# Kernel optimization log

Hardware: AMD Instinct MI355X
Metric: run time of the kernel (lower is better)

Reference implementation:

```python
import jax, jax.numpy as jnp
import numpy as np

NUM_CLASSES = 2
TOP_K = 1500
CONF_THRESH = 0.01
NMS_THRESH = 0.2
VAR0, VAR1 = 0.1, 0.2  # cfg['variance']


def setup_inputs() -> dict:
    key = jax.random.key(0)
    k1, k2, k3 = jax.random.split(key, 3)
    B, P = 32, 76800
    loc_data = jax.random.normal(k1, (B, P, 4), jnp.float32)
    conf_data = jax.random.uniform(k2, (B * P, NUM_CLASSES), jnp.float32)
    prior_data = jax.random.uniform(k3, (P, 4), jnp.float32)
    return {"loc_data": loc_data, "conf_data": conf_data, "prior_data": prior_data}


def _decode(loc, priors):
    # loc, priors: [P,4]; SSD box decode with variances
    cxcy = priors[:, :2] + loc[:, :2] * VAR0 * priors[:, 2:]
    wh = priors[:, 2:] * jnp.exp(loc[:, 2:] * VAR1)
    x1y1 = cxcy - wh * 0.5
    return jnp.concatenate([x1y1, x1y1 + wh], axis=-1)  # [P,4] (x1,y1,x2,y2)


def _nms_per_class(scores, boxes):
    # scores: [P], boxes: [P,4] -> [TOP_K,5] packed (score,x1,y1,x2,y2)
    s = jnp.where(scores > CONF_THRESH, scores, -jnp.inf)
    sk, idx = jax.lax.top_k(s, TOP_K)  # torch nms keeps only top_k candidates
    bk = boxes[idx]
    x1, y1, x2, y2 = bk[:, 0], bk[:, 1], bk[:, 2], bk[:, 3]
    area = (x2 - x1) * (y2 - y1)
    iota = jnp.arange(TOP_K)

    def step(active, i):
        # greedy NMS over score-descending candidates
        xx1 = jnp.maximum(x1, x1[i]); yy1 = jnp.maximum(y1, y1[i])
        xx2 = jnp.minimum(x2, x2[i]); yy2 = jnp.minimum(y2, y2[i])
        inter = jnp.maximum(xx2 - xx1, 0.0) * jnp.maximum(yy2 - yy1, 0.0)
        iou = inter / (area + area[i] - inter)
        kept = active[i]
        suppress = (iou > NMS_THRESH) & (iota != i)
        active = jnp.where(kept, active & ~suppress, active)
        return active, kept

    _, keep = jax.lax.scan(step, sk > -jnp.inf, iota)
    rows = jnp.where(keep[:, None], jnp.concatenate([sk[:, None], bk], axis=1), 0.0)
    # pack kept rows at the front (score-descending order), zeros after
    rank = jnp.cumsum(keep) - 1
    dest = jnp.where(keep, rank, TOP_K)  # dump non-kept into scratch slot
    return jnp.zeros((TOP_K + 1, 5), bk.dtype).at[dest].set(rows)[:TOP_K]


def reference(loc_data, conf_data, prior_data):
    B, P, _ = loc_data.shape
    conf = conf_data.reshape(B, P, NUM_CLASSES)
    decoded = jax.vmap(_decode, in_axes=(0, None))(loc_data, prior_data)  # [B,P,4]
    outs = []
    for cl in range(1, NUM_CLASSES):  # background class 0 stays zero
        outs.append(jax.vmap(_nms_per_class)(conf[:, :, cl], decoded))
    bg = jnp.zeros((B, 1, TOP_K, 5), decoded.dtype)
    return jnp.concatenate([bg, jnp.stack(outs, axis=1)], axis=1)  # [B,C,TOP_K,5]
```

## Files before the change

kernel.cpp:

```cpp
#include <hip/hip_runtime.h>
#include <stdint.h>

typedef unsigned long long u64;
typedef unsigned int u32;

#define NUM_B 32
#define NUM_P 76800
#define TOPK 1500
#define NBINS 2048
#define CAP 2048
#define NWORDS 24
#define NCHUNK 6
#define HSLICES 16
#define HCHUNK (NUM_P / HSLICES)

__device__ __forceinline__ u32 fbits(float f) { return __float_as_uint(f); }
__device__ __forceinline__ int binOf(float s) {
    int b = (int)(s * (float)NBINS);
    return (b > NBINS - 1) ? NBINS - 1 : b;
}
__device__ __forceinline__ u64 readlane64(u64 v, int l) {
    u32 lo = (u32)__builtin_amdgcn_readlane((int)(u32)(v & 0xffffffffu), l);
    u32 hi = (u32)__builtin_amdgcn_readlane((int)(u32)(v >> 32), l);
    return ((u64)hi << 32) | lo;
}

__global__ __launch_bounds__(256) void hist_kernel(const float4* __restrict__ conf4,
                                                   u32* __restrict__ hist,
                                                   u32* __restrict__ bpos) {
    int c = blockIdx.x, b = blockIdx.y, tid = threadIdx.x;
    if (tid < NBINS / HSLICES) bpos[(size_t)b * NBINS + c * (NBINS / HSLICES) + tid] = 0;
    __shared__ u32 h[NBINS];
    for (int i = tid; i < NBINS; i += 256) h[i] = 0;
    __syncthreads();
    const float4* base = conf4 + (size_t)b * (NUM_P / 2) + (size_t)c * (HCHUNK / 2);
    for (int i = tid; i < HCHUNK / 2; i += 256) {
        float4 v = base[i];
        if (v.y > 0.01f) atomicAdd(&h[binOf(v.y)], 1u);
        if (v.w > 0.01f) atomicAdd(&h[binOf(v.w)], 1u);
    }
    __syncthreads();
    u32* outp = hist + ((size_t)b * HSLICES + c) * NBINS;
    for (int i = tid; i < NBINS; i += 256) outp[i] = h[i];
}

__global__ void thresh_kernel(const u32* __restrict__ hist, int* __restrict__ tbin,
                              u32* __restrict__ binbase, u32* __restrict__ bincnt,
                              u32* __restrict__ ntotal) {
    int b = blockIdx.x;
    int tid = threadIdx.x;
    const u32* hb = hist + (size_t)b * HSLICES * NBINS;
    __shared__ u32 vals[256];
    __shared__ int s_min;
    u32 total = 0;
    for (int c = 0; c < NBINS / 256; ++c) {
        if (tid == 0) s_min = 256;
        int bin = NBINS - 1 - (c * 256 + tid);
        u32 v = 0;
#pragma unroll
        for (int s = 0; s < HSLICES; ++s) v += hb[(size_t)s * NBINS + bin];
        __syncthreads();
        vals[tid] = v;
        __syncthreads();
        for (int off = 1; off < 256; off <<= 1) {
            u32 add = (tid >= off) ? vals[tid - off] : 0;
            __syncthreads();
            vals[tid] += add;
            __syncthreads();
        }
        u32 cum = total + vals[tid];
        binbase[(size_t)b * NBINS + bin] = cum - v;
        bincnt [(size_t)b * NBINS + bin] = v;
        if (cum >= TOPK) atomicMin(&s_min, tid);
        __syncthreads();
        if (s_min < 256) {
            if (tid == s_min) { tbin[b] = bin; ntotal[b] = cum; }
            return;
        }
        total += vals[255];
    }
    if (tid == 0) { tbin[b] = 0; ntotal[b] = total; }
}

__global__ __launch_bounds__(256) void compact_kernel(
    const float4* __restrict__ conf4, const int* __restrict__ tbin,
    const u32* __restrict__ binbase, u32* __restrict__ bpos,
    u64* __restrict__ keys) {
    int b = blockIdx.y;
    int tid = threadIdx.x;
    int f4 = blockIdx.x * 256 + tid;
    float4 c = conf4[(size_t)b * (NUM_P / 2) + f4];
    int tb = tbin[b];
    int p0 = f4 * 2, p1 = p0 + 1;

    int b0 = binOf(c.y);
    if (c.y > 0.01f && b0 >= tb) {
        u32 slot = atomicAdd(&bpos[(size_t)b * NBINS + b0], 1u);
        u32 pos = binbase[(size_t)b * NBINS + b0] + slot;
        if (pos < CAP) keys[(size_t)b * CAP + pos] = ((u64)fbits(c.y) << 32) | (u32)(~p0);
    }
    int b1 = binOf(c.w);
    if (c.w > 0.01f && b1 >= tb) {
        u32 slot = atomicAdd(&bpos[(size_t)b * NBINS + b1], 1u);
        u32 pos = binbase[(size_t)b * NBINS + b1] + slot;
        if (pos < CAP) keys[(size_t)b * CAP + pos] = ((u64)fbits(c.w) << 32) | (u32)(~p1);
    }
}

__global__ __launch_bounds__(256) void rank_decode_kernel(
    const u64* __restrict__ keys, const u32* __restrict__ binbase,
    const u32* __restrict__ bincnt, const u32* __restrict__ ntotal,
    const float* __restrict__ loc, const float* __restrict__ prior,
    float* __restrict__ sscore, float* __restrict__ sbox) {
#pragma clang fp contract(off)
    int b = blockIdx.y;
    int g = blockIdx.x * 256 + threadIdx.x;
    int n = (int)min(ntotal[b], (u32)CAP);
    if (g >= n) return;
    const u64* kb = keys + (size_t)b * CAP;
    u64 mykey = kb[g];
    float sc = __uint_as_float((u32)(mykey >> 32));
    int bn = binOf(sc);
    u32 start = binbase[(size_t)b * NBINS + bn];
    u32 end = start + bincnt[(size_t)b * NBINS + bn];
    if (end > (u32)n) end = (u32)n;
    u32 rank = start;
#pragma unroll 4
    for (u32 j = start; j < end; ++j) rank += (kb[j] > mykey) ? 1u : 0u;

    if (rank < TOPK) {
        u32 pidx = ~(u32)mykey;
        const float* lp = &loc[((size_t)b * NUM_P + pidx) * 4];
        const float* pp = &prior[(size_t)pidx * 4];
        float lx = lp[0], ly = lp[1], lw = lp[2], lh = lp[3];
        float pcx = pp[0], pcy = pp[1], pw = pp[2], ph = pp[3];
        float cx = pcx + (lx * 0.1f) * pw;
        float cy = pcy + (ly * 0.1f) * ph;
        float w  = pw * expf(lw * 0.2f);
        float h  = ph * expf(lh * 0.2f);
        float x1 = cx - w * 0.5f;
        float y1 = cy - h * 0.5f;
        float x2 = x1 + w;
        float y2 = y1 + h;
        sscore[(size_t)b * TOPK + rank] = sc;
        float* bx = &sbox[((size_t)b * TOPK + rank) * 4];
        bx[0] = x1; bx[1] = y1; bx[2] = x2; bx[3] = y2;
    }
}

__global__ __launch_bounds__(256) void mask_kernel(
    const float* __restrict__ sbox, u64* __restrict__ mask) {
#pragma clang fp contract(off)
    int w = blockIdx.x, c = blockIdx.y, b = blockIdx.z, tid = threadIdx.x;
    int i = c * 256 + tid;
    if ((w * 64 + 63) <= (c * 256)) return;
    __shared__ float4 cbox[64];
    __shared__ float car[64];
    if (tid < 64) {
        int j = w * 64 + tid;
        float4 bx = make_float4(0.f, 0.f, 0.f, 0.f);
        if (j < TOPK) bx = ((const float4*)sbox)[(size_t)b * TOPK + j];
        cbox[tid] = bx;
        car[tid] = (bx.z - bx.x) * (bx.w - bx.y);
    }
    __syncthreads();
    if (i < TOPK && (i >> 6) <= w) {
        const double MID = 0.5 * ((double)__uint_as_float(0x3E4CCCCDu) +
                                  (double)__uint_as_float(0x3E4CCCCEu));
        const float4 bx = ((const float4*)sbox)[(size_t)b * TOPK + i];
        float x1i = bx.x, y1i = bx.y, x2i = bx.z, y2i = bx.w;
        float ai = (x2i - x1i) * (y2i - y1i);
        u64 m = 0;
        for (int j2 = 0; j2 < 64; ++j2) {
            float4 cb = cbox[j2];
            float xx1 = fmaxf(cb.x, x1i);
            float yy1 = fmaxf(cb.y, y1i);
            float xx2 = fminf(cb.z, x2i);
            float yy2 = fminf(cb.w, y2i);
            float iw = fmaxf(xx2 - xx1, 0.0f);
            float ih = fmaxf(yy2 - yy1, 0.0f);
            float inter = iw * ih;
            float denom = (car[j2] + ai) - inter;
            if ((double)inter >= MID * (double)denom) m |= (1ULL << j2);
        }
        u64 sel = ((i >> 6) == w) ? ((1ULL << (i - w * 64)) - 1ULL) : ~0ULL;
        mask[((size_t)b * NWORDS + w) * TOPK + i] = m & sel;
    }
}

__global__ __launch_bounds__(256) void sweep_kernel(
    const u64* __restrict__ mask, const float* __restrict__ sscore,
    const float* __restrict__ sbox, float* __restrict__ out) {
    int b = blockIdx.x, tid = threadIdx.x;
    int lane = tid & 63, wid = tid >> 6;

    const u64* mbase = mask + (size_t)b * NWORDS * TOPK;

    __shared__ u64 rowbuf[3][NWORDS][65];
    __shared__ u64 aw[NWORDS];
    __shared__ u32 pfx[NWORDS + 1];

    u64 act = 0;
    u64 sv[8];
    if (wid == 0) {
        for (int c = 0; c < NWORDS; ++c) {
            int r = c * 64 + lane;
            bool v = (r < TOPK) && (sscore[(size_t)b * TOPK + r] > 0.0f);
            u64 m = __ballot(v);
            if (lane == c) act = m;
        }
    } else {
        int w0 = (wid - 1) * 8;
#pragma unroll
        for (int t = 0; t < 2; ++t) {
            u64 tmp[8];
#pragma unroll
            for (int k = 0; k < 8; ++k)
                tmp[k] = (w0 + k >= t) ? mbase[(size_t)(w0 + k) * TOPK + t * 64 + lane] : 0ULL;
#pragma unroll
            for (int k = 0; k < 8; ++k)
                rowbuf[t][w0 + k][lane] = tmp[k];
        }
        {
            int rr = 2 * 64 + lane;
#pragma unroll
            for (int k = 0; k < 8; ++k)
                sv[k] = (w0 + k >= 2) ? mbase[(size_t)(w0 + k) * TOPK + rr] : 0ULL;
        }
    }
    __syncthreads();

    for (int T = 0; T < NWORDS; ++T) {
        if (wid == 0) {
            u64 col = rowbuf[T % 3][T][lane];
            u64 actw = readlane64(act, T);
            u64 alive = actw, kept = 0;
            while (alive) {
                int i2 = __ffsll(alive) - 1;
                kept |= (1ULL << i2);
                alive &= ~(1ULL << i2);
                u64 killm = __ballot(((col >> i2) & 1ULL) != 0ULL);
                alive &= ~killm;
            }
            if (lane == T) act = kept;
            if (lane > T && lane < NWORDS) {
                u64 kb = kept;
                while (kb) {
                    int r = __ffsll(kb) - 1;
                    kb &= kb - 1;
                    act &= ~rowbuf[T % 3][lane][r];
                }
            }
        } else {
            int tw = T + 2;
            if (tw < NWORDS) {
                int w0 = (wid - 1) * 8;
#pragma unroll
                for (int k = 0; k < 8; ++k)
                    rowbuf[tw % 3][w0 + k][lane] = sv[k];
                int tn = T + 3;
                if (tn < NWORDS) {
                    int rr = tn * 64 + lane;
                    bool vr = rr < TOPK;
#pragma unroll
                    for (int k = 0; k < 8; ++k)
                        sv[k] = (vr && (w0 + k >= tn))
                                    ? mbase[(size_t)(w0 + k) * TOPK + rr] : 0ULL;
                }
            }
        }
        __syncthreads();
    }

    if (wid == 0 && lane < NWORDS) aw[lane] = act;
    {
        float4* pz = (float4*)(out + (size_t)b * 2 * TOPK * 5);
        float4 z4 = make_float4(0.f, 0.f, 0.f, 0.f);
        for (int t = tid; t < (2 * TOPK * 5) / 4; t += 256) pz[t] = z4;
    }
    __syncthreads();
    if (tid == 0) {
        u32 acc = 0;
        for (int wd = 0; wd < NWORDS; ++wd) { pfx[wd] = acc; acc += (u32)__popcll(aw[wd]); }
        pfx[NWORDS] = acc;
    }
    __syncthreads();
    for (int r = tid; r < TOPK; r += 256) {
        int wd = r >> 6;
        u64 word = aw[wd];
        if ((word >> (r & 63)) & 1ULL) {
            u32 rank = pfx[wd] + (u32)__popcll(word & ((1ULL << (r & 63)) - 1ULL));
            float sc = sscore[(size_t)b * TOPK + r];
            float4 bx = ((const float4*)sbox)[(size_t)b * TOPK + r];
            size_t base_o = (((size_t)b * 2 + 1) * TOPK + (size_t)rank) * 5;
            out[base_o + 0] = sc;
            out[base_o + 1] = bx.x;
            out[base_o + 2] = bx.y;
            out[base_o + 3] = bx.z;
            out[base_o + 4] = bx.w;
        }
    }
}

extern "C" void kernel_launch(void* const* d_in, const int* in_sizes, int n_in,
                              void* d_out, int out_size, void* d_ws, size_t ws_size,
                              hipStream_t stream) {
    const float* loc   = (const float*)d_in[0];
    const float* conf  = (const float*)d_in[1];
    const float* prior = (const float*)d_in[2];
    float* out = (float*)d_out;
    char* ws = (char*)d_ws;

    u64* mask_buf = (u64*)(ws + 0);
    u32* hist     = (u32*)(ws + 0);
    u32* binbase  = (u32*)(ws + 4194304);
    u32* bincnt   = (u32*)(ws + 4456448);
    u32* bpos     = (u32*)(ws + 4718592);
    u64* keys     = (u64*)(ws + 4980736);
    int* tbin     = (int*)(ws + 5505024);
    u32* ntotal   = (u32*)(ws + 5505152);
    float* sscore = (float*)(ws + 9216000);
    float* sbox   = (float*)(ws + 9408000);

    hist_kernel<<<dim3(HSLICES, 32), 256, 0, stream>>>((const float4*)conf, hist, bpos);
    thresh_kernel<<<32, 256, 0, stream>>>(hist, tbin, binbase, bincnt, ntotal);
    compact_kernel<<<dim3(150, 32), 256, 0, stream>>>((const float4*)conf, tbin, binbase,
                                                      bpos, keys);
    rank_decode_kernel<<<dim3(CAP / 256, 32), 256, 0, stream>>>(keys, binbase, bincnt,
                                                                ntotal, loc, prior,
                                                                sscore, sbox);
    mask_kernel<<<dim3(NWORDS, NCHUNK, 32), 256, 0, stream>>>(sbox, mask_buf);
    sweep_kernel<<<32, 256, 0, stream>>>(mask_buf, sscore, sbox, out);
}
```

Measured before the change: 177.1 us.

## Transpose NMS mask to lower-triangular layout and stage it fully in LDS

```diff
diff --git a/kernel.cpp b/kernel.cpp
--- a/kernel.cpp
+++ b/kernel.cpp
@@ -13,16 +13,12 @@
 #define NCHUNK 6
 #define HSLICES 16
 #define HCHUNK (NUM_P / HSLICES)
+#define COLSZ 18336
 
 __device__ __forceinline__ u32 fbits(float f) { return __float_as_uint(f); }
 __device__ __forceinline__ int binOf(float s) {
     int b = (int)(s * (float)NBINS);
     return (b > NBINS - 1) ? NBINS - 1 : b;
-}
-__device__ __forceinline__ u64 readlane64(u64 v, int l) {
-    u32 lo = (u32)__builtin_amdgcn_readlane((int)(u32)(v & 0xffffffffu), l);
-    u32 hi = (u32)__builtin_amdgcn_readlane((int)(u32)(v >> 32), l);
-    return ((u64)hi << 32) | lo;
 }
 
 __global__ __launch_bounds__(256) void hist_kernel(const float4* __restrict__ conf4,
@@ -153,7 +149,7 @@
 #pragma clang fp contract(off)
     int w = blockIdx.x, c = blockIdx.y, b = blockIdx.z, tid = threadIdx.x;
     int i = c * 256 + tid;
-    if ((w * 64 + 63) <= (c * 256)) return;
+    if (w * 64 >= (c + 1) * 256) return;
     __shared__ float4 cbox[64];
     __shared__ float car[64];
     if (tid < 64) {
@@ -164,7 +160,7 @@
         car[tid] = (bx.z - bx.x) * (bx.w - bx.y);
     }
     __syncthreads();
-    if (i < TOPK && (i >> 6) <= w) {
+    if (i < TOPK && w <= (i >> 6)) {
         const double MID = 0.5 * ((double)__uint_as_float(0x3E4CCCCDu) +
                                   (double)__uint_as_float(0x3E4CCCCEu));
         const float4 bx = ((const float4*)sbox)[(size_t)b * TOPK + i];
@@ -183,7 +179,7 @@
             float denom = (car[j2] + ai) - inter;
             if ((double)inter >= MID * (double)denom) m |= (1ULL << j2);
         }
-        u64 sel = ((i >> 6) == w) ? ((1ULL << (i - w * 64)) - 1ULL) : ~0ULL;
+        u64 sel = (w == (i >> 6)) ? ((1ULL << (i - w * 64)) - 1ULL) : ~0ULL;
         mask[((size_t)b * NWORDS + w) * TOPK + i] = m & sel;
     }
 }
@@ -194,90 +190,88 @@
     int b = blockIdx.x, tid = threadIdx.x;
     int lane = tid & 63, wid = tid >> 6;
 
-    const u64* mbase = mask + (size_t)b * NWORDS * TOPK;
-
-    __shared__ u64 rowbuf[3][NWORDS][65];
+    const u64* mb = mask + (size_t)b * NWORDS * TOPK;
+
+    __shared__ u64 col[COLSZ + 64];
     __shared__ u64 aw[NWORDS];
     __shared__ u32 pfx[NWORDS + 1];
 
-    u64 act = 0;
-    u64 sv[8];
-    if (wid == 0) {
-        for (int c = 0; c < NWORDS; ++c) {
-            int r = c * 64 + lane;
-            bool v = (r < TOPK) && (sscore[(size_t)b * TOPK + r] > 0.0f);
-            u64 m = __ballot(v);
-            if (lane == c) act = m;
-        }
-    } else {
-        int w0 = (wid - 1) * 8;
-#pragma unroll
-        for (int t = 0; t < 2; ++t) {
-            u64 tmp[8];
-#pragma unroll
-            for (int k = 0; k < 8; ++k)
-                tmp[k] = (w0 + k >= t) ? mbase[(size_t)(w0 + k) * TOPK + t * 64 + lane] : 0ULL;
-#pragma unroll
-            for (int k = 0; k < 8; ++k)
-                rowbuf[t][w0 + k][lane] = tmp[k];
-        }
-        {
-            int rr = 2 * 64 + lane;
-#pragma unroll
-            for (int k = 0; k < 8; ++k)
-                sv[k] = (w0 + k >= 2) ? mbase[(size_t)(w0 + k) * TOPK + rr] : 0ULL;
-        }
-    }
-    __syncthreads();
-
+    {
+        float4* pz = (float4*)(out + (size_t)b * 2 * TOPK * 5);
+        float4 z4 = make_float4(0.f, 0.f, 0.f, 0.f);
+        for (int t2 = tid; t2 < (2 * TOPK * 5) / 4; t2 += 256) pz[t2] = z4;
+    }
+
+    {
+        u64 A[6], B[6];
+#pragma unroll
+        for (int j = 0; j < 6; ++j) {
+            int r = tid + 256 * j;
+            A[j] = (r < TOPK) ? mb[r] : 0ULL;
+        }
+        for (int T = 0; T < NWORDS; ++T) {
+            if (T + 1 < NWORDS) {
+#pragma unroll
+                for (int j = 0; j < 6; ++j) {
+                    int r = 64 * (T + 1) + tid + 256 * j;
+                    B[j] = (r < TOPK) ? mb[(size_t)(T + 1) * TOPK + r] : 0ULL;
+                }
+            }
+            int base = T * (1532 - 32 * T) + tid;
+#pragma unroll
+            for (int j = 0; j < 6; ++j) {
+                int r = 64 * T + tid + 256 * j;
+                if (r < TOPK) col[base + 256 * j] = A[j];
+            }
+#pragma unroll
+            for (int j = 0; j < 6; ++j) A[j] = B[j];
+        }
+    }
+
+    u32 alivem = 0;
+    {
+        float sv[6];
+#pragma unroll
+        for (int k = 0; k < 6; ++k) {
+            int r = tid + 256 * k;
+            sv[k] = (r < TOPK) ? sscore[(size_t)b * TOPK + r] : 0.0f;
+        }
+#pragma unroll
+        for (int k = 0; k < 6; ++k)
+            if (sv[k] > 0.0f) alivem |= (1u << k);
+    }
+    __syncthreads();
+
+#pragma unroll 1
     for (int T = 0; T < NWORDS; ++T) {
-        if (wid == 0) {
-            u64 col = rowbuf[T % 3][T][lane];
-            u64 actw = readlane64(act, T);
-            u64 alive = actw, kept = 0;
+        if (wid == (T & 3)) {
+            int k = T >> 2;
+            int r = T * 64 + lane;
+            u64 mycol = (r < TOPK) ? col[T * (1532 - 32 * T) + lane] : 0ULL;
+            u64 alive = __ballot(((alivem >> k) & 1u) != 0u);
+            u64 kept = 0;
             while (alive) {
                 int i2 = __ffsll(alive) - 1;
                 kept |= (1ULL << i2);
                 alive &= ~(1ULL << i2);
-                u64 killm = __ballot(((col >> i2) & 1ULL) != 0ULL);
-                alive &= ~killm;
+                alive &= ~__ballot(((mycol >> i2) & 1ULL) != 0ULL);
             }
-            if (lane == T) act = kept;
-            if (lane > T && lane < NWORDS) {
-                u64 kb = kept;
-                while (kb) {
-                    int r = __ffsll(kb) - 1;
-                    kb &= kb - 1;
-                    act &= ~rowbuf[T % 3][lane][r];
-                }
+            alivem = (alivem & ~(1u << k)) | ((u32)((kept >> lane) & 1ULL) << k);
+            if (lane == 0) aw[T] = kept;
+        }
+        __syncthreads();
+        u64 kept = aw[T];
+        int sbase = T * (1532 - 32 * T) - 64 * T + tid;
+#pragma unroll
+        for (int k = 0; k < 6; ++k) {
+            int r = tid + 256 * k;
+            if (r < TOPK && (wid + 4 * k) > T) {
+                u64 cw = col[sbase + 256 * k];
+                if (cw & kept) alivem &= ~(1u << k);
             }
-        } else {
-            int tw = T + 2;
-            if (tw < NWORDS) {
-                int w0 = (wid - 1) * 8;
-#pragma unroll
-                for (int k = 0; k < 8; ++k)
-                    rowbuf[tw % 3][w0 + k][lane] = sv[k];
-                int tn = T + 3;
-                if (tn < NWORDS) {
-                    int rr = tn * 64 + lane;
-                    bool vr = rr < TOPK;
-#pragma unroll
-                    for (int k = 0; k < 8; ++k)
-                        sv[k] = (vr && (w0 + k >= tn))
-                                    ? mbase[(size_t)(w0 + k) * TOPK + rr] : 0ULL;
-                }
-            }
-        }
-        __syncthreads();
-    }
-
-    if (wid == 0 && lane < NWORDS) aw[lane] = act;
-    {
-        float4* pz = (float4*)(out + (size_t)b * 2 * TOPK * 5);
-        float4 z4 = make_float4(0.f, 0.f, 0.f, 0.f);
-        for (int t = tid; t < (2 * TOPK * 5) / 4; t += 256) pz[t] = z4;
-    }
+        }
+    }
+
     __syncthreads();
     if (tid == 0) {
         u32 acc = 0;
```

Result: slower. 182.2 us (+2.9%).

## Stage top-bin candidates during histogram to skip second conf scan in compact

Applied to the files above, without the earlier changes.

```diff
diff --git a/kernel.cpp b/kernel.cpp
--- a/kernel.cpp
+++ b/kernel.cpp
@@ -13,6 +13,8 @@
 #define NCHUNK 6
 #define HSLICES 16
 #define HCHUNK (NUM_P / HSLICES)
+#define PB 1984
+#define SCAP 512
 
 __device__ __forceinline__ u32 fbits(float f) { return __float_as_uint(f); }
 __device__ __forceinline__ int binOf(float s) {
@@ -27,21 +29,47 @@
 
 __global__ __launch_bounds__(256) void hist_kernel(const float4* __restrict__ conf4,
                                                    u32* __restrict__ hist,
-                                                   u32* __restrict__ bpos) {
+                                                   u32* __restrict__ bpos,
+                                                   u64* __restrict__ skey,
+                                                   u32* __restrict__ scnt) {
     int c = blockIdx.x, b = blockIdx.y, tid = threadIdx.x;
     if (tid < NBINS / HSLICES) bpos[(size_t)b * NBINS + c * (NBINS / HSLICES) + tid] = 0;
     __shared__ u32 h[NBINS];
+    __shared__ u64 stg[SCAP];
+    __shared__ u32 sc_s;
+    if (tid == 0) sc_s = 0;
     for (int i = tid; i < NBINS; i += 256) h[i] = 0;
     __syncthreads();
     const float4* base = conf4 + (size_t)b * (NUM_P / 2) + (size_t)c * (HCHUNK / 2);
+    int pbase = c * HCHUNK;
     for (int i = tid; i < HCHUNK / 2; i += 256) {
         float4 v = base[i];
-        if (v.y > 0.01f) atomicAdd(&h[binOf(v.y)], 1u);
-        if (v.w > 0.01f) atomicAdd(&h[binOf(v.w)], 1u);
+        int p0 = pbase + i * 2;
+        if (v.y > 0.01f) {
+            int bn = binOf(v.y);
+            atomicAdd(&h[bn], 1u);
+            if (bn >= PB) {
+                u32 s = atomicAdd(&sc_s, 1u);
+                if (s < SCAP) stg[s] = ((u64)fbits(v.y) << 32) | (u32)(~p0);
+            }
+        }
+        if (v.w > 0.01f) {
+            int bn = binOf(v.w);
+            atomicAdd(&h[bn], 1u);
+            if (bn >= PB) {
+                u32 s = atomicAdd(&sc_s, 1u);
+                if (s < SCAP) stg[s] = ((u64)fbits(v.w) << 32) | (u32)(~(p0 + 1));
+            }
+        }
     }
     __syncthreads();
     u32* outp = hist + ((size_t)b * HSLICES + c) * NBINS;
     for (int i = tid; i < NBINS; i += 256) outp[i] = h[i];
+    u32 n = sc_s;
+    if (tid == 0) scnt[b * HSLICES + c] = n;
+    u64* sk = skey + (size_t)(b * HSLICES + c) * SCAP;
+    u32 nn = (n < (u32)SCAP) ? n : (u32)SCAP;
+    for (u32 i = tid; i < nn; i += 256) sk[i] = stg[i];
 }
 
 __global__ void thresh_kernel(const u32* __restrict__ hist, int* __restrict__ tbin,
@@ -85,14 +113,36 @@
 __global__ __launch_bounds__(256) void compact_kernel(
     const float4* __restrict__ conf4, const int* __restrict__ tbin,
     const u32* __restrict__ binbase, u32* __restrict__ bpos,
-    u64* __restrict__ keys) {
+    u64* __restrict__ keys, const u64* __restrict__ skey,
+    const u32* __restrict__ scnt) {
     int b = blockIdx.y;
     int tid = threadIdx.x;
+    int tb = tbin[b];
+    if (tb >= PB) {
+        bool ovf = false;
+#pragma unroll
+        for (int s = 0; s < HSLICES; ++s) ovf |= (scnt[b * HSLICES + s] > (u32)SCAP);
+        if (!ovf) {
+            if (blockIdx.x >= HSLICES) return;
+            int sl = blockIdx.x;
+            u32 cnt = scnt[b * HSLICES + sl];
+            const u64* sk = skey + (size_t)(b * HSLICES + sl) * SCAP;
+            for (u32 i = tid; i < cnt; i += 256) {
+                u64 key = sk[i];
+                float sc = __uint_as_float((u32)(key >> 32));
+                int bn = binOf(sc);
+                if (bn >= tb) {
+                    u32 slot = atomicAdd(&bpos[(size_t)b * NBINS + bn], 1u);
+                    u32 pos = binbase[(size_t)b * NBINS + bn] + slot;
+                    if (pos < CAP) keys[(size_t)b * CAP + pos] = key;
+                }
+            }
+            return;
+        }
+    }
     int f4 = blockIdx.x * 256 + tid;
     float4 c = conf4[(size_t)b * (NUM_P / 2) + f4];
-    int tb = tbin[b];
     int p0 = f4 * 2, p1 = p0 + 1;
-
     int b0 = binOf(c.y);
     if (c.y > 0.01f && b0 >= tb) {
         u32 slot = atomicAdd(&bpos[(size_t)b * NBINS + b0], 1u);
@@ -319,13 +369,16 @@
     u64* keys     = (u64*)(ws + 4980736);
     int* tbin     = (int*)(ws + 5505024);
     u32* ntotal   = (u32*)(ws + 5505152);
+    u64* skey     = (u64*)(ws + 5505280);
+    u32* scnt     = (u32*)(ws + 7602432);
     float* sscore = (float*)(ws + 9216000);
     float* sbox   = (float*)(ws + 9408000);
 
-    hist_kernel<<<dim3(HSLICES, 32), 256, 0, stream>>>((const float4*)conf, hist, bpos);
+    hist_kernel<<<dim3(HSLICES, 32), 256, 0, stream>>>((const float4*)conf, hist, bpos,
+                                                       skey, scnt);
     thresh_kernel<<<32, 256, 0, stream>>>(hist, tbin, binbase, bincnt, ntotal);
     compact_kernel<<<dim3(150, 32), 256, 0, stream>>>((const float4*)conf, tbin, binbase,
-                                                      bpos, keys);
+                                                      bpos, keys, skey, scnt);
     rank_decode_kernel<<<dim3(CAP / 256, 32), 256, 0, stream>>>(keys, binbase, bincnt,
                                                                 ntotal, loc, prior,
                                                                 sscore, sbox);
```

New measurement: 167.2 us (median of 2 runs). 5.6% less time.
